# Performance work log

Measured on AMD Instinct MI355X. Metric: run time of the kernel, lower is better.

Reference implementation:

```python
import jax, jax.numpy as jnp
import numpy as np

B, L, D, H = 8, 2048, 1024, 1024

def setup_inputs() -> dict:
    key = jax.random.key(0)
    ks = jax.random.split(key, 9)
    s = 1.0 / np.sqrt(H)
    return {
        "input_a": jax.random.normal(ks[0], (B, L, D), jnp.float32),
        "input_b": jax.random.normal(ks[1], (B, L, D), jnp.float32),
        "Wa": jax.random.uniform(ks[2], (H, D), jnp.float32, -s, s),
        "ba": jax.random.uniform(ks[3], (H,), jnp.float32, -s, s),
        "Wb": jax.random.uniform(ks[4], (H, D), jnp.float32, -s, s),
        "bb": jax.random.uniform(ks[5], (H,), jnp.float32, -s, s),
        "Wab": jax.random.uniform(ks[6], (H, H), jnp.float32, -s, s),
        "bab": jax.random.uniform(ks[7], (H,), jnp.float32, -s, s),
        "Wba": jax.random.uniform(ks[8], (H, H), jnp.float32, -s, s),
    }

def reference(input_a, input_b, Wa, ba, Wb, bb, Wab, bab, Wba):
    # projections (torch Linear: x @ W.T + b)
    mapped_a = jnp.einsum('bld,hd->blh', input_a, Wa) + ba  # [B,L,H]
    mapped_b = jnp.einsum('bld,hd->blh', input_b, Wb) + bb  # [B,L,H]
    scores = jnp.einsum('blh,bmh->blm', mapped_a, mapped_b)  # [B,La,Lb]
    attn_a = jax.nn.softmax(scores, axis=-1)                 # softmax over Lb
    attn_b = jax.nn.softmax(scores.swapaxes(1, 2), axis=-1)  # [B,Lb,La], softmax over La
    output_a = jnp.matmul(attn_b, input_b)                   # [B,Lb,Db]
    output_b = jnp.matmul(attn_a.swapaxes(1, 2), input_a)    # [B,Lb,Da]
    output_ab = (jnp.einsum('blh,oh->blo', output_a, Wab) + bab
                 + jnp.einsum('blh,oh->blo', output_b, Wba))
    return (output_a, output_b, output_ab)
```

## Files before the change

kernel.cpp:

```cpp
#include <hip/hip_runtime.h>

typedef _Float16 f16;
typedef __attribute__((ext_vector_type(8))) _Float16 f16x8;
typedef __attribute__((ext_vector_type(4))) float f32x4v;

#define DEVI __device__ __forceinline__

DEVI unsigned short f2h_bits(float x) {
    _Float16 h = (_Float16)x;
    return __builtin_bit_cast(unsigned short, h);
}

DEVI void stage128(f16* lds, const f16* g, int ld, int w, int lane) {
#pragma unroll
    for (int j = 0; j < 4; ++j) {
        int q   = j * 256 + w * 64 + lane;
        int row = q >> 3;
        int c   = q & 7;
        int cs  = c ^ (row & 7);
        const f16* src = g + (size_t)row * ld + cs * 8;
        f16* dst = lds + q * 8;
        __builtin_amdgcn_global_load_lds((const __attribute__((address_space(1))) void*)src,
                                         (__attribute__((address_space(3))) void*)dst, 16, 0, 0);
    }
}

DEVI f16x8 read_frag(const f16* lds, int row, int kbyte) {
    int off = row * 128 + (kbyte ^ ((row & 7) << 4));
    return *(const f16x8*)((const char*)lds + off);
}

#define MFMA(a, b, c) __builtin_amdgcn_mfma_f32_16x16x32_f16(a, b, c, 0, 0, 0)

__global__ __launch_bounds__(256) void gemm_bt(
    const f16* __restrict__ A, const f16* __restrict__ B,
    const float* __restrict__ bias, const float* __restrict__ rowScale,
    float* __restrict__ Cf, int ldc, long batchC,
    f16* __restrict__ Ch, int ldcH, long batchCh, int colOff,
    int K, int lda, int ldb, long batchA, long batchB, int outMode)
{
    __shared__ f16 As[128 * 64];
    __shared__ f16 Bs[128 * 64];
    const int z = blockIdx.z;
    const f16* Ab = A + (size_t)z * batchA + (size_t)blockIdx.y * 128 * lda;
    const f16* Bb = B + (size_t)z * batchB + (size_t)blockIdx.x * 128 * ldb;
    const int t = threadIdx.x, w = t >> 6, lane = t & 63;
    const int r = lane & 15, h = lane >> 4;
    const int wr = w >> 1, wc = w & 1;
    f32x4v acc[4][4] = {};

#pragma unroll 1
    for (int k0 = 0; k0 < K; k0 += 64) {
        stage128(As, Ab + k0, lda, w, lane);
        stage128(Bs, Bb + k0, ldb, w, lane);
        __syncthreads();
#pragma unroll
        for (int kk = 0; kk < 2; ++kk) {
            const int kb = kk * 64 + h * 16;
            f16x8 a[4], b[4];
#pragma unroll
            for (int mi = 0; mi < 4; ++mi) a[mi] = read_frag(As, wr * 64 + mi * 16 + r, kb);
#pragma unroll
            for (int ni = 0; ni < 4; ++ni) b[ni] = read_frag(Bs, wc * 64 + ni * 16 + r, kb);
#pragma unroll
            for (int mi = 0; mi < 4; ++mi)
#pragma unroll
                for (int ni = 0; ni < 4; ++ni)
                    acc[mi][ni] = MFMA(a[mi], b[ni], acc[mi][ni]);
        }
        __syncthreads();
    }

    const int m0 = blockIdx.y * 128 + wr * 64;
    const int n0 = blockIdx.x * 128 + wc * 64;
#pragma unroll
    for (int ni = 0; ni < 4; ++ni) {
        const int col = n0 + ni * 16 + r;
        const float bv = bias ? bias[col] : 0.f;
#pragma unroll
        for (int mi = 0; mi < 4; ++mi) {
#pragma unroll
            for (int tt = 0; tt < 4; ++tt) {
                const int row = m0 + mi * 16 + h * 4 + tt;
                float v = acc[mi][ni][tt] + bv;
                if (rowScale) v *= rowScale[(size_t)z * 2048 + row];
                if (outMode & 1) Cf[(size_t)z * batchC + (size_t)row * ldc + col] = v;
                if (outMode & 2) Ch[(size_t)z * batchCh + (size_t)row * ldcH + colOff + col] = (f16)v;
            }
        }
    }
}

__global__ __launch_bounds__(256) void transpose_cast(
    const float* __restrict__ in, f16* __restrict__ plain, f16* __restrict__ tr)
{
    __shared__ unsigned short tile[64][72];
    const int z = blockIdx.z, l0 = blockIdx.y * 64, d0 = blockIdx.x * 64;
    const int t = threadIdx.x, r = t >> 4, c4 = (t & 15) * 4;
#pragma unroll
    for (int rep = 0; rep < 4; ++rep) {
        const int l = rep * 16 + r;
        const size_t gi = ((size_t)z * 2048 + l0 + l) * 1024 + d0 + c4;
        const f32x4v v = *(const f32x4v*)&in[gi];
        ushort4 u = make_ushort4(f2h_bits(v[0]), f2h_bits(v[1]), f2h_bits(v[2]), f2h_bits(v[3]));
        *(ushort4*)&plain[gi] = u;
        tile[c4 + 0][l] = u.x;
        tile[c4 + 1][l] = u.y;
        tile[c4 + 2][l] = u.z;
        tile[c4 + 3][l] = u.w;
    }
    __syncthreads();
#pragma unroll
    for (int rep = 0; rep < 4; ++rep) {
        const int d = rep * 16 + r;
        ushort4 u = make_ushort4(tile[d][c4 + 0], tile[d][c4 + 1], tile[d][c4 + 2], tile[d][c4 + 3]);
        *(ushort4*)&tr[((size_t)z * 1024 + d0 + d) * 2048 + l0 + c4] = u;
    }
}

__global__ void cast_w(const float* __restrict__ in, f16* __restrict__ out) {
    const int i = (blockIdx.x * 256 + threadIdx.x) * 4;
    f32x4v v = *(const f32x4v*)&in[i];
    *(ushort4*)&out[i] = make_ushort4(f2h_bits(v[0]), f2h_bits(v[1]), f2h_bits(v[2]), f2h_bits(v[3]));
}

__global__ void cast_cat(const float* __restrict__ wab, const float* __restrict__ wba,
                         f16* __restrict__ out) {
    const int i = (blockIdx.x * 256 + threadIdx.x) * 4;
    const int row = i >> 10, col = i & 1023;
    f32x4v va = *(const f32x4v*)&wab[i];
    f32x4v vb = *(const f32x4v*)&wba[i];
    *(ushort4*)&out[(size_t)row * 2048 + col] =
        make_ushort4(f2h_bits(va[0]), f2h_bits(va[1]), f2h_bits(va[2]), f2h_bits(va[3]));
    *(ushort4*)&out[(size_t)row * 2048 + 1024 + col] =
        make_ushort4(f2h_bits(vb[0]), f2h_bits(vb[1]), f2h_bits(vb[2]), f2h_bits(vb[3]));
}

template <typename T>
DEVI void load8_row(const T* p, int t, float* x);
template <>
DEVI void load8_row<float>(const float* p, int t, float* x) {
    const f32x4v v0 = *(const f32x4v*)&p[t * 4];
    const f32x4v v1 = *(const f32x4v*)&p[1024 + t * 4];
#pragma unroll
    for (int j = 0; j < 4; ++j) { x[j] = v0[j]; x[4 + j] = v1[j]; }
}
template <>
DEVI void load8_row<f16>(const f16* p, int t, float* x) {
    const f16x8 v = *(const f16x8*)&p[t * 8];
#pragma unroll
    for (int j = 0; j < 8; ++j) x[j] = (float)v[j];
}

template <typename T>
__global__ __launch_bounds__(256) void row_stats(const T* __restrict__ ST,
                                                 float* __restrict__ cmax,
                                                 float* __restrict__ csumInv)
{
    const size_t row = blockIdx.x;
    const T* p = ST + row * 2048;
    const int t = threadIdx.x, wid = t >> 6, lane = t & 63;
    float x[8];
    load8_row<T>(p, t, x);
    float m = x[0];
#pragma unroll
    for (int j = 1; j < 8; ++j) m = fmaxf(m, x[j]);
    for (int off = 32; off; off >>= 1) m = fmaxf(m, __shfl_xor(m, off));
    __shared__ float red[8];
    if (lane == 0) red[wid] = m;
    __syncthreads();
    m = fmaxf(fmaxf(red[0], red[1]), fmaxf(red[2], red[3]));
    float s = 0.f;
#pragma unroll
    for (int j = 0; j < 8; ++j) s += __expf(x[j] - m);
    for (int off = 32; off; off >>= 1) s += __shfl_xor(s, off);
    if (lane == 0) red[4 + wid] = s;
    __syncthreads();
    if (t == 0) {
        cmax[row] = m;
        csumInv[row] = 1.f / (red[4] + red[5] + red[6] + red[7]);
    }
}

template <typename T>
__global__ __launch_bounds__(256) void col_part(const T* __restrict__ ST,
                                                float* __restrict__ pmax,
                                                float* __restrict__ psum)
{
    const int z = blockIdx.z, mc = blockIdx.y;
    const int col = blockIdx.x * 256 + threadIdx.x;
    const T* p = ST + ((size_t)z * 2048 + (size_t)mc * 64) * 2048 + col;
    float m = -1e30f;
#pragma unroll 8
    for (int i = 0; i < 64; ++i) m = fmaxf(m, (float)p[(size_t)i * 2048]);
    float s = 0.f;
#pragma unroll 8
    for (int i = 0; i < 64; ++i) s += __expf((float)p[(size_t)i * 2048] - m);
    const size_t o = ((size_t)z * 32 + mc) * 2048 + col;
    pmax[o] = m;
    psum[o] = s;
}

__global__ void col_fin(const float* __restrict__ pmax, const float* __restrict__ psum,
                        float* __restrict__ rmax, float* __restrict__ rsumInv)
{
    const int g = blockIdx.x * 256 + threadIdx.x;
    const int z = g >> 11, col = g & 2047;
    const float* pm = pmax + (size_t)z * 32 * 2048 + col;
    const float* ps = psum + (size_t)z * 32 * 2048 + col;
    float m = -1e30f;
#pragma unroll
    for (int i = 0; i < 32; ++i) m = fmaxf(m, pm[(size_t)i * 2048]);
    float s = 0.f;
#pragma unroll
    for (int i = 0; i < 32; ++i) s += ps[(size_t)i * 2048] * __expf(pm[(size_t)i * 2048] - m);
    rmax[g] = m;
    rsumInv[g] = 1.f / s;
}

template <typename T>
DEVI void load8_g(const T* p, float* x);
template <>
DEVI void load8_g<float>(const float* p, float* x) {
    const f32x4v v0 = *(const f32x4v*)p;
    const f32x4v v1 = *(const f32x4v*)(p + 4);
#pragma unroll
    for (int j = 0; j < 4; ++j) { x[j] = v0[j]; x[4 + j] = v1[j]; }
}
template <>
DEVI void load8_g<f16>(const f16* p, float* x) {
    const f16x8 v = *(const f16x8*)p;
#pragma unroll
    for (int j = 0; j < 8; ++j) x[j] = (float)v[j];
}

template <typename T>
__global__ __launch_bounds__(256) void exp_p(const T* __restrict__ ST,
                                             const float* __restrict__ cmax,
                                             const float* __restrict__ rmax,
                                             const float* __restrict__ rsumInv,
                                             f16* __restrict__ Pa, f16* __restrict__ Pb)
{
    const size_t g = ((size_t)blockIdx.x * 256 + threadIdx.x) * 8;
    const int row = (int)(g >> 11);
    const int z = row >> 11;
    const int l = (int)(g & 2047);
    const float cm = cmax[row];
    const float* rm = rmax + ((size_t)z << 11) + l;
    const float* ri = rsumInv + ((size_t)z << 11) + l;
    float x[8];
    load8_g<T>(ST + g, x);
    const f32x4v rm0 = *(const f32x4v*)rm, rm1 = *(const f32x4v*)(rm + 4);
    const f32x4v ri0 = *(const f32x4v*)ri, ri1 = *(const f32x4v*)(ri + 4);
    f16x8 pa, pb;
#pragma unroll
    for (int j = 0; j < 4; ++j) {
        pa[j]     = (f16)__expf(x[j] - cm);
        pa[4 + j] = (f16)__expf(x[4 + j] - cm);
        pb[j]     = (f16)(__expf(x[j] - rm0[j]) * ri0[j]);
        pb[4 + j] = (f16)(__expf(x[4 + j] - rm1[j]) * ri1[j]);
    }
    *(f16x8*)(Pa + g) = pa;
    *(f16x8*)(Pb + g) = pb;
}

extern "C" void kernel_launch(void* const* d_in, const int* in_sizes, int n_in,
                              void* d_out, int out_size, void* d_ws, size_t ws_size,
                              hipStream_t stream) {
    const float* in_a = (const float*)d_in[0];
    const float* in_b = (const float*)d_in[1];
    const float* Wa   = (const float*)d_in[2];
    const float* ba   = (const float*)d_in[3];
    const float* Wb   = (const float*)d_in[4];
    const float* bb   = (const float*)d_in[5];
    const float* Wab  = (const float*)d_in[6];
    const float* bab  = (const float*)d_in[7];
    const float* Wba  = (const float*)d_in[8];

    const size_t MB = 1u << 20;
    char* ws = (char*)d_ws;
    f16*   aT  = (f16*)(ws + 0 * MB);
    f16*   bT  = (f16*)(ws + 32 * MB);
    f16*   PaT = (f16*)(ws + 64 * MB);
    f16*   PbT = (f16*)(ws + 128 * MB);
    f16*   aB  = (f16*)(ws + 64 * MB);
    f16*   bB  = (f16*)(ws + 96 * MB);
    f16*   maH = (f16*)(ws + 128 * MB);
    f16*   mbH = (f16*)(ws + 160 * MB);
    float* STf = (float*)(ws + 192 * MB);
    f16*   STh = (f16*)(ws + 192 * MB);
    f16*   catH = (f16*)(ws + 192 * MB);

    const bool useF32 = ws_size >= 334 * MB;
    char* woff = ws + 192 * MB + (useF32 ? 128 : 64) * MB;
    f16*   WaH   = (f16*)(woff + 0 * MB);
    f16*   WbH   = (f16*)(woff + 2 * MB);
    f16*   WcatH = (f16*)(woff + 4 * MB);
    float* cmaxP = (float*)(woff + 8 * MB);
    float* csumIP= (float*)(woff + 8 * MB + 64 * 1024);
    float* rmaxP = (float*)(woff + 8 * MB + 128 * 1024);
    float* rsumIP= (float*)(woff + 8 * MB + 192 * 1024);
    float* pmaxP = (float*)(woff + 9 * MB);
    float* psumP = (float*)(woff + 11 * MB);

    float* outA  = (float*)d_out;
    float* outB  = outA + 16777216;
    float* outAB = outB + 16777216;

    dim3 blk(256);
    const long LL = 2048L * 2048L, LD = 2048L * 1024L;

    transpose_cast<<<dim3(16, 32, 8), blk, 0, stream>>>(in_a, aB, aT);
    transpose_cast<<<dim3(16, 32, 8), blk, 0, stream>>>(in_b, bB, bT);
    cast_w<<<dim3(1024), blk, 0, stream>>>(Wa, WaH);
    cast_w<<<dim3(1024), blk, 0, stream>>>(Wb, WbH);
    cast_cat<<<dim3(1024), blk, 0, stream>>>(Wab, Wba, WcatH);

    gemm_bt<<<dim3(8, 128, 1), blk, 0, stream>>>(aB, WaH, ba, nullptr,
                                                 nullptr, 0, 0, maH, 1024, 0, 0,
                                                 1024, 1024, 1024, 0, 0, 2);
    gemm_bt<<<dim3(8, 128, 1), blk, 0, stream>>>(bB, WbH, bb, nullptr,
                                                 nullptr, 0, 0, mbH, 1024, 0, 0,
                                                 1024, 1024, 1024, 0, 0, 2);
    if (useF32) {
        gemm_bt<<<dim3(16, 16, 8), blk, 0, stream>>>(mbH, maH, nullptr, nullptr,
                                                     STf, 2048, LL, nullptr, 0, 0, 0,
                                                     1024, 1024, 1024, LD, LD, 1);
        row_stats<float><<<dim3(16384), blk, 0, stream>>>(STf, cmaxP, csumIP);
        col_part<float><<<dim3(8, 32, 8), blk, 0, stream>>>(STf, pmaxP, psumP);
        col_fin<<<dim3(64), blk, 0, stream>>>(pmaxP, psumP, rmaxP, rsumIP);
        exp_p<float><<<dim3(16384), blk, 0, stream>>>(STf, cmaxP, rmaxP, rsumIP, PaT, PbT);
    } else {
        gemm_bt<<<dim3(16, 16, 8), blk, 0, stream>>>(mbH, maH, nullptr, nullptr,
                                                     nullptr, 0, 0, STh, 2048, LL, 0,
                                                     1024, 1024, 1024, LD, LD, 2);
        row_stats<f16><<<dim3(16384), blk, 0, stream>>>(STh, cmaxP, csumIP);
        col_part<f16><<<dim3(8, 32, 8), blk, 0, stream>>>(STh, pmaxP, psumP);
        col_fin<<<dim3(64), blk, 0, stream>>>(pmaxP, psumP, rmaxP, rsumIP);
        exp_p<f16><<<dim3(16384), blk, 0, stream>>>(STh, cmaxP, rmaxP, rsumIP, PaT, PbT);
    }

    gemm_bt<<<dim3(8, 16, 8), blk, 0, stream>>>(PaT, bT, nullptr, csumIP,
                                                outA, 1024, LD, catH, 2048, LL, 0,
                                                2048, 2048, 2048, LL, LD, 3);
    gemm_bt<<<dim3(8, 16, 8), blk, 0, stream>>>(PbT, aT, nullptr, nullptr,
                                                outB, 1024, LD, catH, 2048, LL, 1024,
                                                2048, 2048, 2048, LL, LD, 3);

    gemm_bt<<<dim3(8, 128, 1), blk, 0, stream>>>(catH, WcatH, bab, nullptr,
                                                 outAB, 1024, 0, nullptr, 0, 0, 0,
                                                 2048, 2048, 2048, 0, 0, 1);

    (void)in_sizes; (void)n_in; (void)out_size; (void)ws_size;
}
```

Baseline: 1.022 ms.

## Replace 128x128 GEMM with double-buffered 256x256 pipelined kernel and XCD remap

Swaps the simple 128x128 single-buffered GEMM for a 256x256-tile, 512-thread kernel. It double-buffers LDS and interleaves quarter-tile async global-to-LDS loads with MFMA phases, using manual vmcnt waits, raw barriers and setprio. It also remaps workgroup IDs so consecutive tiles land on the same XCD. The aims are to hide load latency behind compute, raise data reuse per tile, and improve L2 locality. The trade-offs are much higher register and LDS pressure, fewer workgroups for the small GEMMs, and fragile hand-tuned synchronization.

```diff
diff --git a/kernel.cpp b/kernel.cpp
--- a/kernel.cpp
+++ b/kernel.cpp
@@ -11,19 +11,13 @@
     return __builtin_bit_cast(unsigned short, h);
 }
 
-DEVI void stage128(f16* lds, const f16* g, int ld, int w, int lane) {
-#pragma unroll
-    for (int j = 0; j < 4; ++j) {
-        int q   = j * 256 + w * 64 + lane;
-        int row = q >> 3;
-        int c   = q & 7;
-        int cs  = c ^ (row & 7);
-        const f16* src = g + (size_t)row * ld + cs * 8;
-        f16* dst = lds + q * 8;
-        __builtin_amdgcn_global_load_lds((const __attribute__((address_space(1))) void*)src,
-                                         (__attribute__((address_space(3))) void*)dst, 16, 0, 0);
-    }
-}
+DEVI void wgbar() {
+    asm volatile("" ::: "memory");
+    __builtin_amdgcn_s_barrier();
+    asm volatile("" ::: "memory");
+}
+DEVI void vmwait4() { asm volatile("s_waitcnt vmcnt(4)" ::: "memory"); }
+DEVI void vmwait0() { asm volatile("s_waitcnt vmcnt(0)" ::: "memory"); }
 
 DEVI f16x8 read_frag(const f16* lds, int row, int kbyte) {
     int off = row * 128 + (kbyte ^ ((row & 7) << 4));
@@ -32,60 +26,131 @@
 
 #define MFMA(a, b, c) __builtin_amdgcn_mfma_f32_16x16x32_f16(a, b, c, 0, 0, 0)
 
-__global__ __launch_bounds__(256) void gemm_bt(
+DEVI void stage_Aq(f16* ldsA, const f16* g, int ld, int q, int w, int lane) {
+#pragma unroll
+    for (int p = 0; p < 2; ++p) {
+        const int qi = w * 64 + lane;
+        const int grow = p * 128 + q * 64 + (qi >> 3);
+        const int c = qi & 7;
+        const f16* src = g + (size_t)grow * ld + ((c ^ (grow & 7)) * 8);
+        f16* dst = ldsA + grow * 64 + c * 8;
+        __builtin_amdgcn_global_load_lds((const __attribute__((address_space(1))) void*)src,
+                                         (__attribute__((address_space(3))) void*)dst, 16, 0, 0);
+    }
+}
+DEVI void stage_Bq(f16* ldsB, const f16* g, int ld, int q, int w, int lane) {
+#pragma unroll
+    for (int j = 0; j < 2; ++j) {
+        const int qi = (w * 2 + j) * 64 + lane;
+        const int grow = (qi >> 8) * 64 + q * 32 + ((qi >> 3) & 31);
+        const int c = qi & 7;
+        const f16* src = g + (size_t)grow * ld + ((c ^ (grow & 7)) * 8);
+        f16* dst = ldsB + grow * 64 + c * 8;
+        __builtin_amdgcn_global_load_lds((const __attribute__((address_space(1))) void*)src,
+                                         (__attribute__((address_space(3))) void*)dst, 16, 0, 0);
+    }
+}
+
+__global__ __launch_bounds__(512, 2) void gemm256(
     const f16* __restrict__ A, const f16* __restrict__ B,
     const float* __restrict__ bias, const float* __restrict__ rowScale,
     float* __restrict__ Cf, int ldc, long batchC,
     f16* __restrict__ Ch, int ldcH, long batchCh, int colOff,
     int K, int lda, int ldb, long batchA, long batchB, int outMode)
 {
-    __shared__ f16 As[128 * 64];
-    __shared__ f16 Bs[128 * 64];
-    const int z = blockIdx.z;
-    const f16* Ab = A + (size_t)z * batchA + (size_t)blockIdx.y * 128 * lda;
-    const f16* Bb = B + (size_t)z * batchB + (size_t)blockIdx.x * 128 * ldb;
+    __shared__ f16 sm[2][2][16384];
+    const int gx = gridDim.x, gy = gridDim.y;
+    const int nwg = gx * gy * (int)gridDim.z;
+    const int flat = blockIdx.x + gx * (blockIdx.y + gy * blockIdx.z);
+    const int id = (flat & 7) * (nwg >> 3) + (flat >> 3);
+    const int bz = id / (gx * gy);
+    const int rem = id % (gx * gy);
+    const int by = rem / gx, bx = rem % gx;
+
+    const f16* Ab = A + (size_t)bz * batchA + (size_t)by * 256 * lda;
+    const f16* Bb = B + (size_t)bz * batchB + (size_t)bx * 256 * ldb;
     const int t = threadIdx.x, w = t >> 6, lane = t & 63;
-    const int r = lane & 15, h = lane >> 4;
-    const int wr = w >> 1, wc = w & 1;
-    f32x4v acc[4][4] = {};
+    const int r = lane & 15, h16 = (lane >> 4) * 16;
+    const int wr = w >> 2, wc = w & 3;
+    f16* A0 = sm[0][0]; f16* B0 = sm[0][1];
+    f16* A1 = sm[1][0]; f16* B1 = sm[1][1];
+    f32x4v acc[8][4] = {};
+    f16x8 a0[4], a1[4], b0[2], b1[2];
+    const int NT = K >> 6, NTm = NT - 1, NI = NT >> 1;
+
+    stage_Aq(A0, Ab, lda, 0, w, lane);
+    stage_Aq(A0, Ab, lda, 1, w, lane);
+    stage_Bq(B0, Bb, ldb, 0, w, lane);
+    stage_Bq(B0, Bb, ldb, 1, w, lane);
+    stage_Aq(A1, Ab + 64, lda, 0, w, lane);
+    stage_Bq(B1, Bb + 64, ldb, 1, w, lane);
+    vmwait4();
+    wgbar();
+
+#define LDA_(LA, QM) _Pragma("unroll") for (int mi = 0; mi < 4; ++mi) { \
+        const int ar = wr * 128 + (QM) * 64 + mi * 16 + r;              \
+        a0[mi] = read_frag(LA, ar, h16); a1[mi] = read_frag(LA, ar, 64 + h16); }
+#define LDB_(LB, QN) _Pragma("unroll") for (int ni = 0; ni < 2; ++ni) { \
+        const int br = wc * 64 + (QN) * 32 + ni * 16 + r;               \
+        b0[ni] = read_frag(LB, br, h16); b1[ni] = read_frag(LB, br, 64 + h16); }
+#define MM_(QM, QN) __builtin_amdgcn_s_setprio(1);                          \
+    _Pragma("unroll") for (int mi = 0; mi < 4; ++mi)                        \
+    _Pragma("unroll") for (int ni = 0; ni < 2; ++ni) {                      \
+        acc[(QM)*4+mi][(QN)*2+ni] = MFMA(a0[mi], b0[ni], acc[(QM)*4+mi][(QN)*2+ni]); \
+        acc[(QM)*4+mi][(QN)*2+ni] = MFMA(a1[mi], b1[ni], acc[(QM)*4+mi][(QN)*2+ni]); } \
+    __builtin_amdgcn_s_setprio(0);
 
 #pragma unroll 1
-    for (int k0 = 0; k0 < K; k0 += 64) {
-        stage128(As, Ab + k0, lda, w, lane);
-        stage128(Bs, Bb + k0, ldb, w, lane);
-        __syncthreads();
-#pragma unroll
-        for (int kk = 0; kk < 2; ++kk) {
-            const int kb = kk * 64 + h * 16;
-            f16x8 a[4], b[4];
-#pragma unroll
-            for (int mi = 0; mi < 4; ++mi) a[mi] = read_frag(As, wr * 64 + mi * 16 + r, kb);
-#pragma unroll
-            for (int ni = 0; ni < 4; ++ni) b[ni] = read_frag(Bs, wc * 64 + ni * 16 + r, kb);
-#pragma unroll
-            for (int mi = 0; mi < 4; ++mi)
-#pragma unroll
-                for (int ni = 0; ni < 4; ++ni)
-                    acc[mi][ni] = MFMA(a[mi], b[ni], acc[mi][ni]);
-        }
-        __syncthreads();
-    }
-
-    const int m0 = blockIdx.y * 128 + wr * 64;
-    const int n0 = blockIdx.x * 128 + wc * 64;
-#pragma unroll
-    for (int ni = 0; ni < 4; ++ni) {
-        const int col = n0 + ni * 16 + r;
+    for (int i = 0; i < NI; ++i) {
+        const f16* At1 = Ab + ((2 * i + 1) & NTm) * 64;
+        const f16* Bt1 = Bb + ((2 * i + 1) & NTm) * 64;
+        const f16* At2 = Ab + ((2 * i + 2) & NTm) * 64;
+        const f16* Bt2 = Bb + ((2 * i + 2) & NTm) * 64;
+        const f16* At3 = Ab + ((2 * i + 3) & NTm) * 64;
+        const f16* Bt3 = Bb + ((2 * i + 3) & NTm) * 64;
+        LDA_(A0, 0); LDB_(B0, 0);
+        stage_Aq(A1, At1, lda, 1, w, lane);
+        wgbar(); MM_(0, 0); wgbar();
+        LDB_(B0, 1);
+        stage_Bq(B1, Bt1, ldb, 0, w, lane);
+        wgbar(); MM_(0, 1); wgbar();
+        LDA_(A0, 1);
+        stage_Aq(A0, At2, lda, 0, w, lane);
+        wgbar(); MM_(1, 1); wgbar();
+        LDB_(B0, 0);
+        stage_Bq(B0, Bt2, ldb, 1, w, lane);
+        wgbar(); MM_(1, 0); vmwait4(); wgbar();
+        LDA_(A1, 0); LDB_(B1, 0);
+        stage_Aq(A0, At2, lda, 1, w, lane);
+        wgbar(); MM_(0, 0); wgbar();
+        LDB_(B1, 1);
+        stage_Bq(B0, Bt2, ldb, 0, w, lane);
+        wgbar(); MM_(0, 1); wgbar();
+        LDA_(A1, 1);
+        stage_Aq(A1, At3, lda, 0, w, lane);
+        wgbar(); MM_(1, 1); wgbar();
+        LDB_(B1, 0);
+        stage_Bq(B1, Bt3, ldb, 1, w, lane);
+        wgbar(); MM_(1, 0); vmwait4(); wgbar();
+    }
+    vmwait0();
+
+    const int m0 = by * 256 + wr * 128;
+    const int n0 = bx * 256 + wc * 64;
+    const int h4 = (lane >> 4) * 4;
+#pragma unroll
+    for (int ni2 = 0; ni2 < 4; ++ni2) {
+        const int col = n0 + ni2 * 16 + r;
         const float bv = bias ? bias[col] : 0.f;
 #pragma unroll
-        for (int mi = 0; mi < 4; ++mi) {
+        for (int mi2 = 0; mi2 < 8; ++mi2) {
 #pragma unroll
             for (int tt = 0; tt < 4; ++tt) {
-                const int row = m0 + mi * 16 + h * 4 + tt;
-                float v = acc[mi][ni][tt] + bv;
-                if (rowScale) v *= rowScale[(size_t)z * 2048 + row];
-                if (outMode & 1) Cf[(size_t)z * batchC + (size_t)row * ldc + col] = v;
-                if (outMode & 2) Ch[(size_t)z * batchCh + (size_t)row * ldcH + colOff + col] = (f16)v;
+                const int row = m0 + mi2 * 16 + h4 + tt;
+                float v = acc[mi2][ni2][tt] + bv;
+                if (rowScale) v *= rowScale[(size_t)bz * 2048 + row];
+                if (outMode & 1) Cf[(size_t)bz * batchC + (size_t)row * ldc + col] = v;
+                if (outMode & 2) Ch[(size_t)bz * batchCh + (size_t)row * ldcH + colOff + col] = (f16)v;
             }
         }
     }
@@ -307,7 +372,7 @@
     float* outB  = outA + 16777216;
     float* outAB = outB + 16777216;
 
-    dim3 blk(256);
+    dim3 blk(256), blk512(512);
     const long LL = 2048L * 2048L, LD = 2048L * 1024L;
 
     transpose_cast<<<dim3(16, 32, 8), blk, 0, stream>>>(in_a, aB, aT);
@@ -316,40 +381,40 @@
     cast_w<<<dim3(1024), blk, 0, stream>>>(Wb, WbH);
     cast_cat<<<dim3(1024), blk, 0, stream>>>(Wab, Wba, WcatH);
 
-    gemm_bt<<<dim3(8, 128, 1), blk, 0, stream>>>(aB, WaH, ba, nullptr,
-                                                 nullptr, 0, 0, maH, 1024, 0, 0,
-                                                 1024, 1024, 1024, 0, 0, 2);
-    gemm_bt<<<dim3(8, 128, 1), blk, 0, stream>>>(bB, WbH, bb, nullptr,
-                                                 nullptr, 0, 0, mbH, 1024, 0, 0,
-                                                 1024, 1024, 1024, 0, 0, 2);
+    gemm256<<<dim3(4, 64, 1), blk512, 0, stream>>>(aB, WaH, ba, nullptr,
+                                                   nullptr, 0, 0, maH, 1024, 0, 0,
+                                                   1024, 1024, 1024, 0, 0, 2);
+    gemm256<<<dim3(4, 64, 1), blk512, 0, stream>>>(bB, WbH, bb, nullptr,
+                                                   nullptr, 0, 0, mbH, 1024, 0, 0,
+                                                   1024, 1024, 1024, 0, 0, 2);
     if (useF32) {
-        gemm_bt<<<dim3(16, 16, 8), blk, 0, stream>>>(mbH, maH, nullptr, nullptr,
-                                                     STf, 2048, LL, nullptr, 0, 0, 0,
-                                                     1024, 1024, 1024, LD, LD, 1);
+        gemm256<<<dim3(8, 8, 8), blk512, 0, stream>>>(mbH, maH, nullptr, nullptr,
+                                                      STf, 2048, LL, nullptr, 0, 0, 0,
+                                                      1024, 1024, 1024, LD, LD, 1);
         row_stats<float><<<dim3(16384), blk, 0, stream>>>(STf, cmaxP, csumIP);
         col_part<float><<<dim3(8, 32, 8), blk, 0, stream>>>(STf, pmaxP, psumP);
         col_fin<<<dim3(64), blk, 0, stream>>>(pmaxP, psumP, rmaxP, rsumIP);
         exp_p<float><<<dim3(16384), blk, 0, stream>>>(STf, cmaxP, rmaxP, rsumIP, PaT, PbT);
     } else {
-        gemm_bt<<<dim3(16, 16, 8), blk, 0, stream>>>(mbH, maH, nullptr, nullptr,
-                                                     nullptr, 0, 0, STh, 2048, LL, 0,
-                                                     1024, 1024, 1024, LD, LD, 2);
+        gemm256<<<dim3(8, 8, 8), blk512, 0, stream>>>(mbH, maH, nullptr, nullptr,
+                                                      nullptr, 0, 0, STh, 2048, LL, 0,
+                                                      1024, 1024, 1024, LD, LD, 2);
         row_stats<f16><<<dim3(16384), blk, 0, stream>>>(STh, cmaxP, csumIP);
         col_part<f16><<<dim3(8, 32, 8), blk, 0, stream>>>(STh, pmaxP, psumP);
         col_fin<<<dim3(64), blk, 0, stream>>>(pmaxP, psumP, rmaxP, rsumIP);
         exp_p<f16><<<dim3(16384), blk, 0, stream>>>(STh, cmaxP, rmaxP, rsumIP, PaT, PbT);
     }
 
-    gemm_bt<<<dim3(8, 16, 8), blk, 0, stream>>>(PaT, bT, nullptr, csumIP,
-                                                outA, 1024, LD, catH, 2048, LL, 0,
-                                                2048, 2048, 2048, LL, LD, 3);
-    gemm_bt<<<dim3(8, 16, 8), blk, 0, stream>>>(PbT, aT, nullptr, nullptr,
-                                                outB, 1024, LD, catH, 2048, LL, 1024,
-                                                2048, 2048, 2048, LL, LD, 3);
-
-    gemm_bt<<<dim3(8, 128, 1), blk, 0, stream>>>(catH, WcatH, bab, nullptr,
-                                                 outAB, 1024, 0, nullptr, 0, 0, 0,
-                                                 2048, 2048, 2048, 0, 0, 1);
+    gemm256<<<dim3(4, 8, 8), blk512, 0, stream>>>(PaT, bT, nullptr, csumIP,
+                                                  outA, 1024, LD, catH, 2048, LL, 0,
+                                                  2048, 2048, 2048, LL, LD, 3);
+    gemm256<<<dim3(4, 8, 8), blk512, 0, stream>>>(PbT, aT, nullptr, nullptr,
+                                                  outB, 1024, LD, catH, 2048, LL, 1024,
+                                                  2048, 2048, 2048, LL, LD, 3);
+
+    gemm256<<<dim3(4, 64, 1), blk512, 0, stream>>>(catH, WcatH, bab, nullptr,
+                                                   outAB, 1024, 0, nullptr, 0, 0, 0,
+                                                   2048, 2048, 2048, 0, 0, 1);
 
     (void)in_sizes; (void)n_in; (void)out_size; (void)ws_size;
 }
```

New measurement: 851.4 us. 16.7% less time.
